# Kernel optimization log

Hardware: AMD Instinct MI355X
Metric: run time of the kernel (lower is better)

## Reference

```python
import jax, jax.numpy as jnp
import numpy as np
from jax import lax

B = 256; C_IN = 12; H = 84; W = 84
HID = 1024; NC = 16; NE = 512; EPC = 64
FLAT = 64 * 7 * 7  # encoder output size for 84x84 input


def setup_inputs() -> dict:
    key = jax.random.key(0)
    ks = jax.random.split(key, 16)
    s = 0.02
    inp = {
        "obs": jax.random.normal(ks[0], (B, C_IN, H, W), dtype=jnp.float32),
        "k1": jax.random.normal(ks[1], (32, C_IN, 8, 8), dtype=jnp.float32) * s,
        "cb1": jnp.zeros((32,), jnp.float32),
        "k2": jax.random.normal(ks[2], (64, 32, 4, 4), dtype=jnp.float32) * s,
        "cb2": jnp.zeros((64,), jnp.float32),
        "k3": jax.random.normal(ks[3], (64, 64, 3, 3), dtype=jnp.float32) * s,
        "cb3": jnp.zeros((64,), jnp.float32),
        "Wproj": jax.random.normal(ks[4], (FLAT, HID), dtype=jnp.float32) * s,
        "bproj": jnp.zeros((HID,), jnp.float32),
        "Wcat": jax.random.normal(ks[5], (HID, NC), dtype=jnp.float32) * s,
        "bcat": jnp.zeros((NC,), jnp.float32),
        "W1": jax.random.normal(ks[6], (NC, HID, HID // 2), dtype=jnp.float32) * s,
        "b1": jnp.zeros((NC, HID // 2), jnp.float32),
        "W2": jax.random.normal(ks[7], (NC, HID // 2, EPC), dtype=jnp.float32) * s,
        "b2": jnp.zeros((NC, EPC), jnp.float32),
        "mapping": jax.random.randint(ks[8], (NC, EPC), 0, NE, dtype=jnp.int64)
        if jax.config.jax_enable_x64 else jax.random.randint(ks[8], (NC, EPC), 0, NE, dtype=jnp.int32),
    }
    return inp


def _conv(x, k, b, stride):
    y = lax.conv_general_dilated(x, k, (stride, stride), "VALID",
                                 dimension_numbers=("NCHW", "OIHW", "NCHW"))
    return y + b[None, :, None, None]


def reference(obs, k1, cb1, k2, cb2, k3, cb3, Wproj, bproj, Wcat, bcat,
              W1, b1, W2, b2, mapping):
    # --- CNN encoder ---
    x = jax.nn.relu(_conv(obs, k1, cb1, 4))   # [B,32,20,20]
    x = jax.nn.relu(_conv(x, k2, cb2, 2))     # [B,64,9,9]
    x = jax.nn.relu(_conv(x, k3, cb3, 1))     # [B,64,7,7]
    feats = x.reshape(x.shape[0], -1)          # [B,3136]

    hidden = jax.nn.relu(feats @ Wproj + bproj)          # [B,HID]
    category_logits = hidden @ Wcat + bcat               # [B,NC]
    category_probs = jax.nn.softmax(category_logits, axis=-1)

    # --- batched per-category expert heads (fused) ---
    h1 = jax.nn.relu(jnp.einsum("bh,chm->bcm", hidden, W1) + b1)   # [B,NC,HID/2]
    local = jax.nn.sigmoid(jnp.einsum("bcm,cme->bce", h1, W2) + b2)  # [B,NC,EPC]
    weighted = category_probs[:, :, None] * local                    # [B,NC,EPC]

    # scatter-add into global expert buffer; mapping [NC,EPC] broadcasts to [B,NC,EPC]
    expert_probs = jnp.zeros((hidden.shape[0], NE), hidden.dtype)
    expert_probs = expert_probs.at[:, mapping].add(weighted)

    return category_logits, expert_probs, hidden
```

## Files before the change

### kernel.cpp

```cpp
#include <hip/hip_runtime.h>
#include <hip/hip_bf16.h>


#define B_    256
#define CIN   12
#define HH    84
#define WW    84
#define HID   1024
#define NC    16
#define NE    512
#define EPC   64
#define FLAT  3136

typedef short short8 __attribute__((ext_vector_type(8)));
typedef short short4_t __attribute__((ext_vector_type(4)));
typedef float f32x4 __attribute__((ext_vector_type(4)));

__device__ __forceinline__ short f2bf(float x) {
    unsigned int u = __float_as_uint(x);
    u = (u + 0x7FFFu + ((u >> 16) & 1u)) >> 16;
    return (short)u;
}

__global__ __launch_bounds__(256) void cast_k1_kernel(
        const float* __restrict__ k1, short* __restrict__ k1bf) {
    int i = blockIdx.x * 256 + threadIdx.x;
    if (i < 32 * 768) k1bf[i] = f2bf(k1[i]);
}

__global__ __launch_bounds__(256) void conv1_mfma_kernel(
        const float* __restrict__ obs, const short* __restrict__ k1bf,
        const float* __restrict__ cb1, float* __restrict__ x1) {
    const int tid = threadIdx.x;
    const int w = tid >> 6, l = tid & 63;
    const int lr = l & 15, g = l >> 4;
    const int mfb = blockIdx.x * 64 + w * 16;

    const int row_a = mfb + lr;
    const int b_a = row_a / 400;
    const int p_a = row_a % 400;
    const int oy = p_a / 20, ox = p_a % 20;
    const float* abase = obs + (size_t)b_a * (CIN * HH * WW) + (4 * oy) * WW + 4 * ox;
    const short* bb0 = k1bf + lr * 768;
    const short* bb1 = k1bf + (16 + lr) * 768;

    f32x4 acc0 = {0.f, 0.f, 0.f, 0.f}, acc1 = {0.f, 0.f, 0.f, 0.f};
    #pragma unroll 4
    for (int s = 0; s < 24; ++s) {
        const int idx = s * 4 + g;
        const int ic = idx >> 3, ky = idx & 7;
        const float* ap = abase + ic * (HH * WW) + ky * WW;
        float4 f0 = *(const float4*)ap;
        float4 f1 = *(const float4*)(ap + 4);
        short8 a;
        a[0] = f2bf(f0.x); a[1] = f2bf(f0.y); a[2] = f2bf(f0.z); a[3] = f2bf(f0.w);
        a[4] = f2bf(f1.x); a[5] = f2bf(f1.y); a[6] = f2bf(f1.z); a[7] = f2bf(f1.w);
        short8 b0 = *(const short8*)(bb0 + s * 32 + g * 8);
        short8 b1 = *(const short8*)(bb1 + s * 32 + g * 8);
        acc0 = __builtin_amdgcn_mfma_f32_16x16x32_bf16(a, b0, acc0, 0, 0, 0);
        acc1 = __builtin_amdgcn_mfma_f32_16x16x32_bf16(a, b1, acc1, 0, 0, 0);
    }
    #pragma unroll
    for (int r = 0; r < 4; ++r) {
        const int ro = mfb + g * 4 + r;
        const int b_o = ro / 400, p_o = ro % 400;
        float* xp = x1 + (size_t)b_o * 32 * 400 + p_o;
        xp[(size_t)lr * 400]        = fmaxf(acc0[r] + cb1[lr], 0.f);
        xp[(size_t)(16 + lr) * 400] = fmaxf(acc1[r] + cb1[16 + lr], 0.f);
    }
}

__global__ __launch_bounds__(288) void conv2_kernel(
        const float* __restrict__ x1, const float* __restrict__ k2,
        const float* __restrict__ cb2, float* __restrict__ x2) {
    __shared__ float slab[32][20][20];
    const int b = blockIdx.x, tid = threadIdx.x;
    const float* src = x1 + (size_t)b * 32 * 400;
    float4* s4 = (float4*)&slab[0][0][0];
    const float4* g4 = (const float4*)src;
    for (int l = tid; l < 3200; l += 288) s4[l] = g4[l];
    __syncthreads();

    const int ocp = tid / 9, oy = tid % 9;
    const int oc0 = 2 * ocp;
    float acc[2][9];
    #pragma unroll
    for (int o = 0; o < 2; ++o) {
        float bv = cb2[oc0 + o];
        #pragma unroll
        for (int i = 0; i < 9; ++i) acc[o][i] = bv;
    }
    for (int ic = 0; ic < 32; ++ic) {
        float wvv[2][16];
        const float* wp = k2 + oc0 * 512 + ic * 16;
        #pragma unroll
        for (int o = 0; o < 2; ++o)
            #pragma unroll
            for (int ky = 0; ky < 4; ++ky) {
                float4 t = *(const float4*)(wp + o * 512 + 4 * ky);
                wvv[o][4*ky] = t.x; wvv[o][4*ky+1] = t.y;
                wvv[o][4*ky+2] = t.z; wvv[o][4*ky+3] = t.w;
            }
        #pragma unroll
        for (int ky = 0; ky < 4; ++ky) {
            const int row = 2 * oy + ky;
            float rf[20];
            const float4* rp = (const float4*)&slab[ic][row][0];
            #pragma unroll
            for (int q = 0; q < 5; ++q) {
                float4 t = rp[q];
                rf[4*q] = t.x; rf[4*q+1] = t.y; rf[4*q+2] = t.z; rf[4*q+3] = t.w;
            }
            #pragma unroll
            for (int ox = 0; ox < 9; ++ox)
                #pragma unroll
                for (int kx = 0; kx < 4; ++kx) {
                    float v = rf[2 * ox + kx];
                    acc[0][ox] += v * wvv[0][4 * ky + kx];
                    acc[1][ox] += v * wvv[1][4 * ky + kx];
                }
        }
    }
    #pragma unroll
    for (int o = 0; o < 2; ++o) {
        float* dst = x2 + ((size_t)(b * 64 + oc0 + o) * 9 + oy) * 9;
        #pragma unroll
        for (int ox = 0; ox < 9; ++ox) dst[ox] = fmaxf(acc[o][ox], 0.f);
    }
}

__global__ __launch_bounds__(224) void conv3_kernel(
        const float* __restrict__ x2, const float* __restrict__ k3,
        const float* __restrict__ cb3, short* __restrict__ featsbf) {
    __shared__ float slab[64][9][12];
    const int b = blockIdx.x, tid = threadIdx.x;
    for (int l = tid; l < 64 * 9 * 12; l += 224) {
        int ic = l / 108, rest = l % 108, r = rest / 12, x = rest % 12;
        slab[ic][r][x] = (x < 9) ? x2[((size_t)(b * 64 + ic) * 9 + r) * 9 + x] : 0.f;
    }
    __syncthreads();

    const int ocp = tid / 7, oy = tid % 7;
    const int oc0 = 2 * ocp;
    float acc[2][7];
    #pragma unroll
    for (int o = 0; o < 2; ++o) {
        float bv = cb3[oc0 + o];
        #pragma unroll
        for (int i = 0; i < 7; ++i) acc[o][i] = bv;
    }
    for (int ic = 0; ic < 64; ++ic) {
        float wv2[2][9];
        const float* wp = k3 + oc0 * 576 + ic * 9;
        #pragma unroll
        for (int j = 0; j < 9; ++j) { wv2[0][j] = wp[j]; wv2[1][j] = wp[576 + j]; }
        #pragma unroll
        for (int ky = 0; ky < 3; ++ky) {
            const int row = oy + ky;
            float rf[12];
            const float4* rp = (const float4*)&slab[ic][row][0];
            #pragma unroll
            for (int q = 0; q < 3; ++q) {
                float4 t = rp[q];
                rf[4*q] = t.x; rf[4*q+1] = t.y; rf[4*q+2] = t.z; rf[4*q+3] = t.w;
            }
            #pragma unroll
            for (int ox = 0; ox < 7; ++ox)
                #pragma unroll
                for (int kx = 0; kx < 3; ++kx) {
                    float v = rf[ox + kx];
                    acc[0][ox] += v * wv2[0][3 * ky + kx];
                    acc[1][ox] += v * wv2[1][3 * ky + kx];
                }
        }
    }
    #pragma unroll
    for (int o = 0; o < 2; ++o) {
        short* dst = featsbf + (size_t)b * FLAT + (oc0 + o) * 49 + oy * 7;
        #pragma unroll
        for (int ox = 0; ox < 7; ++ox) dst[ox] = f2bf(fmaxf(acc[o][ox], 0.f));
    }
}

__global__ __launch_bounds__(256) void proj_mfma_kernel(
        const short* __restrict__ Abf, const float* __restrict__ W,
        float* __restrict__ accum4) {
    __shared__ __align__(16) short lbt[16][40];
    const int tid = threadIdx.x;
    const int w = tid >> 6, l = tid & 63, lr = l & 15, g = l >> 4;
    const int n0 = blockIdx.x * 16;
    const int kz = blockIdx.y;
    const int sb = kz * 24 + (kz < 2 ? kz : 2);
    const int ns = (kz < 2) ? 25 : 24;
    const int krp = tid >> 4, nn = tid & 15;

    f32x4 acc[4] = {};
    const short* arow[4];
    #pragma unroll
    for (int i = 0; i < 4; ++i)
        arow[i] = Abf + (size_t)(w * 64 + i * 16 + lr) * FLAT;

    for (int s = sb; s < sb + ns; ++s) {
        const int k0 = s * 32;
        {
            const float* wp = W + (size_t)(k0 + 2 * krp) * HID + n0 + nn;
            unsigned int lo = (unsigned short)f2bf(wp[0]);
            unsigned int hi = (unsigned short)f2bf(wp[HID]);
            *(unsigned int*)&lbt[nn][2 * krp] = lo | (hi << 16);
        }
        __syncthreads();
        short8 b = *(const short8*)&lbt[lr][g * 8];
        #pragma unroll
        for (int i = 0; i < 4; ++i) {
            short8 a = *(const short8*)(arow[i] + k0 + g * 8);
            acc[i] = __builtin_amdgcn_mfma_f32_16x16x32_bf16(a, b, acc[i], 0, 0, 0);
        }
        __syncthreads();
    }
    float* dst = accum4 + (size_t)kz * (B_ * HID);
    #pragma unroll
    for (int i = 0; i < 4; ++i)
        #pragma unroll
        for (int r = 0; r < 4; ++r)
            dst[(size_t)(w * 64 + i * 16 + g * 4 + r) * HID + n0 + lr] = acc[i][r];
}

__global__ __launch_bounds__(256) void proj_epi2_kernel(
        const float* __restrict__ accum4, const float* __restrict__ bproj,
        float* __restrict__ hidden, short* __restrict__ hbf) {
    const int i = blockIdx.x * 256 + threadIdx.x;
    float4 v = *(const float4*)&accum4[4 * i];
    #pragma unroll
    for (int kz = 1; kz < 4; ++kz) {
        float4 t = *(const float4*)&accum4[(size_t)kz * (B_ * HID) + 4 * i];
        v.x += t.x; v.y += t.y; v.z += t.z; v.w += t.w;
    }
    float4 bb = *(const float4*)&bproj[(4 * i) & (HID - 1)];
    float4 r;
    r.x = fmaxf(v.x + bb.x, 0.f); r.y = fmaxf(v.y + bb.y, 0.f);
    r.z = fmaxf(v.z + bb.z, 0.f); r.w = fmaxf(v.w + bb.w, 0.f);
    *(float4*)&hidden[4 * i] = r;
    short4_t h; h[0] = f2bf(r.x); h[1] = f2bf(r.y); h[2] = f2bf(r.z); h[3] = f2bf(r.w);
    *(short4_t*)&hbf[4 * i] = h;
}

__global__ __launch_bounds__(256) void cat_softmax_kernel(
        const float* __restrict__ hidden, const float* __restrict__ Wcat,
        const float* __restrict__ bcat, float* __restrict__ logits,
        float* __restrict__ probs) {
    __shared__ float red[256];
    __shared__ float lvals[16];
    const int b = blockIdx.x, tid = threadIdx.x;
    const int cc = tid & 15, kq = tid >> 4;
    const float* hrow = hidden + (size_t)b * HID;
    float p = 0.f;
    for (int t = 0; t < 64; ++t) {
        int k = kq * 64 + t;
        p += hrow[k] * Wcat[k * NC + cc];
    }
    red[tid] = p;
    __syncthreads();
    if (tid < 16) {
        float s = bcat[tid];
        #pragma unroll
        for (int q = 0; q < 16; ++q) s += red[q * 16 + tid];
        logits[b * NC + tid] = s;
        lvals[tid] = s;
    }
    __syncthreads();
    if (tid < 16) {
        float m = lvals[0];
        #pragma unroll
        for (int q = 1; q < 16; ++q) m = fmaxf(m, lvals[q]);
        float sum = 0.f;
        #pragma unroll
        for (int q = 0; q < 16; ++q) sum += expf(lvals[q] - m);
        probs[b * NC + tid] = expf(lvals[tid] - m) / sum;
    }
}

__global__ __launch_bounds__(256) void expert1_mfma_kernel(
        const short* __restrict__ Hbf, const float* __restrict__ W1,
        const float* __restrict__ b1, short* __restrict__ h1bf) {
    __shared__ __align__(16) short lbt[32][40];
    const int tid = threadIdx.x;
    const int w = tid >> 6, l = tid & 63, lr = l & 15, g = l >> 4;
    const int n0 = blockIdx.x * 32;
    const int c  = blockIdx.y;
    const float* Wc = W1 + (size_t)c * (HID * (HID / 2));

    f32x4 acc[4][2] = {};
    const short* arow[4];
    #pragma unroll
    for (int i = 0; i < 4; ++i)
        arow[i] = Hbf + (size_t)(w * 64 + i * 16 + lr) * HID;

    for (int s = 0; s < 32; ++s) {
        const int k0 = s * 32;
        #pragma unroll
        for (int it = 0; it < 2; ++it) {
            const int idx = tid + it * 256;
            const int krp = idx >> 5, nn = idx & 31;
            const float* wp = Wc + (size_t)(k0 + 2 * krp) * (HID / 2) + n0 + nn;
            unsigned int lo = (unsigned short)f2bf(wp[0]);
            unsigned int hi = (unsigned short)f2bf(wp[HID / 2]);
            *(unsigned int*)&lbt[nn][2 * krp] = lo | (hi << 16);
        }
        __syncthreads();
        short8 b0 = *(const short8*)&lbt[lr][g * 8];
        short8 b1v = *(const short8*)&lbt[16 + lr][g * 8];
        #pragma unroll
        for (int i = 0; i < 4; ++i) {
            short8 a = *(const short8*)(arow[i] + k0 + g * 8);
            acc[i][0] = __builtin_amdgcn_mfma_f32_16x16x32_bf16(a, b0, acc[i][0], 0, 0, 0);
            acc[i][1] = __builtin_amdgcn_mfma_f32_16x16x32_bf16(a, b1v, acc[i][1], 0, 0, 0);
        }
        __syncthreads();
    }
    #pragma unroll
    for (int i = 0; i < 4; ++i)
        #pragma unroll
        for (int j = 0; j < 2; ++j)
            #pragma unroll
            for (int r = 0; r < 4; ++r) {
                const int m = w * 64 + i * 16 + g * 4 + r;
                const int col = n0 + j * 16 + lr;
                float v = fmaxf(acc[i][j][r] + b1[c * (HID / 2) + col], 0.f);
                h1bf[((size_t)c * B_ + m) * (HID / 2) + col] = f2bf(v);
            }
}

__global__ __launch_bounds__(256) void expert2_mfma_kernel(
        const short* __restrict__ h1bf, const float* __restrict__ W2,
        const float* __restrict__ b2, const float* __restrict__ probs,
        const int* __restrict__ mapping, float* __restrict__ outexp) {
    __shared__ __align__(16) short lbt[64][40];
    const int tid = threadIdx.x;
    const int w = tid >> 6, l = tid & 63, lr = l & 15, g = l >> 4;
    const int mfb = blockIdx.x * 16;
    const int c = blockIdx.y;
    const float* Wc = W2 + (size_t)c * ((HID / 2) * EPC);
    const short* arow = h1bf + ((size_t)c * B_ + mfb + lr) * (HID / 2);

    f32x4 acc = {};
    for (int s = 0; s < 16; ++s) {
        const int k0 = s * 32;
        #pragma unroll
        for (int it = 0; it < 4; ++it) {
            const int idx = tid + it * 256;
            const int krp = idx >> 6, nn = idx & 63;
            const float* wp = Wc + (size_t)(k0 + 2 * krp) * EPC + nn;
            unsigned int lo = (unsigned short)f2bf(wp[0]);
            unsigned int hi = (unsigned short)f2bf(wp[EPC]);
            *(unsigned int*)&lbt[nn][2 * krp] = lo | (hi << 16);
        }
        __syncthreads();
        short8 b = *(const short8*)&lbt[w * 16 + lr][g * 8];
        short8 a = *(const short8*)(arow + k0 + g * 8);
        acc = __builtin_amdgcn_mfma_f32_16x16x32_bf16(a, b, acc, 0, 0, 0);
        __syncthreads();
    }
    const int e = w * 16 + lr;
    const float bb = b2[c * EPC + e];
    const int tgt = mapping[c * EPC + e];
    #pragma unroll
    for (int r = 0; r < 4; ++r) {
        const int m = mfb + g * 4 + r;
        const float lg = acc[r] + bb;
        const float v = probs[m * NC + c] / (1.f + expf(-lg));
        atomicAdd(&outexp[(size_t)m * NE + tgt], v);
    }
}

extern "C" void kernel_launch(void* const* d_in, const int* in_sizes, int n_in,
                              void* d_out, int out_size, void* d_ws, size_t ws_size,
                              hipStream_t stream) {
    const float* obs   = (const float*)d_in[0];
    const float* k1    = (const float*)d_in[1];
    const float* cb1   = (const float*)d_in[2];
    const float* k2    = (const float*)d_in[3];
    const float* cb2   = (const float*)d_in[4];
    const float* k3    = (const float*)d_in[5];
    const float* cb3   = (const float*)d_in[6];
    const float* Wproj = (const float*)d_in[7];
    const float* bproj = (const float*)d_in[8];
    const float* Wcat  = (const float*)d_in[9];
    const float* bcat  = (const float*)d_in[10];
    const float* W1    = (const float*)d_in[11];
    const float* b1    = (const float*)d_in[12];
    const float* W2    = (const float*)d_in[13];
    const float* b2    = (const float*)d_in[14];
    const int*   mapping = (const int*)d_in[15];

    float* out    = (float*)d_out;
    float* logits = out;
    float* outexp = out + B_ * NC;
    float* hidden = out + B_ * NC + B_ * NE;

    char* ws = (char*)d_ws;
    float* x1      = (float*)ws;
    float* accum4  = (float*)ws;
    short* h1bf    = (short*)(ws + 4194304);
    short* hidbf   = (short*)(ws + 8388608);
    float* x2      = (float*)(ws + 13107200);
    short* featsbf = (short*)(ws + 18415616);
    float* probs   = (float*)(ws + 20021248);
    short* k1bf    = (short*)(ws + 20037632);

    hipMemsetAsync(outexp, 0, (size_t)B_ * NE * sizeof(float), stream);

    cast_k1_kernel<<<dim3(96), 256, 0, stream>>>(k1, k1bf);
    conv1_mfma_kernel<<<dim3(1600), 256, 0, stream>>>(obs, k1bf, cb1, x1);
    conv2_kernel<<<dim3(B_), 288, 0, stream>>>(x1, k2, cb2, x2);
    conv3_kernel<<<dim3(B_), 224, 0, stream>>>(x2, k3, cb3, featsbf);
    proj_mfma_kernel<<<dim3(64, 4), 256, 0, stream>>>(featsbf, Wproj, accum4);
    proj_epi2_kernel<<<dim3(256), 256, 0, stream>>>(accum4, bproj, hidden, hidbf);
    cat_softmax_kernel<<<dim3(B_), 256, 0, stream>>>(hidden, Wcat, bcat, logits, probs);
    expert1_mfma_kernel<<<dim3(16, 16), 256, 0, stream>>>(hidbf, W1, b1, h1bf);
    expert2_mfma_kernel<<<dim3(16, 16), 256, 0, stream>>>(h1bf, W2, b2, probs, mapping, outexp);
}
```

Before: 408.8 us.

## Move all convs to MFMA with NHWC bf16 activations and pre-transposed bf16 weights

```diff
diff --git a/kernel.cpp b/kernel.cpp
--- a/kernel.cpp
+++ b/kernel.cpp
@@ -22,25 +22,64 @@
     return (short)u;
 }
 
-__global__ __launch_bounds__(256) void cast_k1_kernel(
-        const float* __restrict__ k1, short* __restrict__ k1bf) {
+__global__ __launch_bounds__(256) void prep_weights_kernel(
+        const float* __restrict__ k1, const float* __restrict__ k2,
+        const float* __restrict__ k3, short* __restrict__ k1bf,
+        short* __restrict__ k2t, short* __restrict__ k3t) {
     int i = blockIdx.x * 256 + threadIdx.x;
-    if (i < 32 * 768) k1bf[i] = f2bf(k1[i]);
-}
-
-__global__ __launch_bounds__(256) void conv1_mfma_kernel(
+    if (i < 24576) {
+        k1bf[i] = f2bf(k1[i]);
+    } else if (i < 24576 + 32768) {
+        int j = i - 24576;
+        int oc = j >> 9, rem = j & 511, tap = rem >> 5, ic = rem & 31;
+        k2t[j] = f2bf(k2[oc * 512 + ic * 16 + tap]);
+    } else if (i < 24576 + 32768 + 36864) {
+        int j = i - 57344;
+        int oc = j / 576, rem = j % 576, tap = rem >> 6, ic = rem & 63;
+        k3t[j] = f2bf(k3[oc * 576 + ic * 9 + tap]);
+    }
+}
+
+__global__ __launch_bounds__(256) void transpose_cast_kernel(
+        const float* __restrict__ src, short* __restrict__ dst,
+        int R, int C, long sbs, long dbs) {
+    __shared__ float tile[32][33];
+    const int c0 = blockIdx.x * 32, r0 = blockIdx.y * 32, z = blockIdx.z;
+    const int tx = threadIdx.x & 31, ty = threadIdx.x >> 5;
+    const float* s = src + (size_t)z * sbs;
+    short* d = dst + (size_t)z * dbs;
+    #pragma unroll
+    for (int it = 0; it < 4; ++it)
+        tile[ty + it * 8][tx] = s[(size_t)(r0 + ty + it * 8) * C + c0 + tx];
+    __syncthreads();
+    #pragma unroll
+    for (int it = 0; it < 4; ++it) {
+        int j = ty + it * 8;
+        d[(size_t)(c0 + j) * R + r0 + tx] = f2bf(tile[tx][j]);
+    }
+}
+
+__global__ __launch_bounds__(448) void conv1_mfma_kernel(
         const float* __restrict__ obs, const short* __restrict__ k1bf,
-        const float* __restrict__ cb1, float* __restrict__ x1) {
+        const float* __restrict__ cb1, short* __restrict__ x1bf) {
+    __shared__ short slab[CIN][24][88];
+    const int oyq = blockIdx.x, b = blockIdx.y;
     const int tid = threadIdx.x;
-    const int w = tid >> 6, l = tid & 63;
-    const int lr = l & 15, g = l >> 4;
-    const int mfb = blockIdx.x * 64 + w * 16;
-
-    const int row_a = mfb + lr;
-    const int b_a = row_a / 400;
-    const int p_a = row_a % 400;
-    const int oy = p_a / 20, ox = p_a % 20;
-    const float* abase = obs + (size_t)b_a * (CIN * HH * WW) + (4 * oy) * WW + 4 * ox;
+
+    const float* src = obs + (size_t)b * (CIN * HH * WW) + (20 * oyq) * WW;
+    for (int l = tid; l < CIN * 24 * 21; l += 448) {
+        int ic = l / 504, rem = l % 504, r = rem / 21, c4 = rem % 21;
+        float4 f = *(const float4*)(src + (size_t)ic * (HH * WW) + r * WW + 4 * c4);
+        short4_t v;
+        v[0] = f2bf(f.x); v[1] = f2bf(f.y); v[2] = f2bf(f.z); v[3] = f2bf(f.w);
+        *(short4_t*)&slab[ic][r][4 * c4] = v;
+    }
+    __syncthreads();
+
+    const int w = tid >> 6, l = tid & 63, lr = l & 15, g = l >> 4;
+    const int p = w * 16 + lr;
+    const int pw = (p < 100) ? p : 99;
+    const int oy_l = pw / 20, ox = pw % 20;
     const short* bb0 = k1bf + lr * 768;
     const short* bb1 = k1bf + (16 + lr) * 768;
 
@@ -49,199 +88,130 @@
     for (int s = 0; s < 24; ++s) {
         const int idx = s * 4 + g;
         const int ic = idx >> 3, ky = idx & 7;
-        const float* ap = abase + ic * (HH * WW) + ky * WW;
-        float4 f0 = *(const float4*)ap;
-        float4 f1 = *(const float4*)(ap + 4);
+        const short* ap = &slab[ic][4 * oy_l + ky][4 * ox];
         short8 a;
-        a[0] = f2bf(f0.x); a[1] = f2bf(f0.y); a[2] = f2bf(f0.z); a[3] = f2bf(f0.w);
-        a[4] = f2bf(f1.x); a[5] = f2bf(f1.y); a[6] = f2bf(f1.z); a[7] = f2bf(f1.w);
+        *(short4_t*)&a       = *(const short4_t*)ap;
+        *((short4_t*)&a + 1) = *(const short4_t*)(ap + 4);
         short8 b0 = *(const short8*)(bb0 + s * 32 + g * 8);
         short8 b1 = *(const short8*)(bb1 + s * 32 + g * 8);
         acc0 = __builtin_amdgcn_mfma_f32_16x16x32_bf16(a, b0, acc0, 0, 0, 0);
         acc1 = __builtin_amdgcn_mfma_f32_16x16x32_bf16(a, b1, acc1, 0, 0, 0);
     }
+    const float c0v = cb1[lr], c1v = cb1[16 + lr];
     #pragma unroll
     for (int r = 0; r < 4; ++r) {
-        const int ro = mfb + g * 4 + r;
-        const int b_o = ro / 400, p_o = ro % 400;
-        float* xp = x1 + (size_t)b_o * 32 * 400 + p_o;
-        xp[(size_t)lr * 400]        = fmaxf(acc0[r] + cb1[lr], 0.f);
-        xp[(size_t)(16 + lr) * 400] = fmaxf(acc1[r] + cb1[16 + lr], 0.f);
-    }
-}
-
-__global__ __launch_bounds__(288) void conv2_kernel(
-        const float* __restrict__ x1, const float* __restrict__ k2,
-        const float* __restrict__ cb2, float* __restrict__ x2) {
-    __shared__ float slab[32][20][20];
-    const int b = blockIdx.x, tid = threadIdx.x;
-    const float* src = x1 + (size_t)b * 32 * 400;
-    float4* s4 = (float4*)&slab[0][0][0];
-    const float4* g4 = (const float4*)src;
-    for (int l = tid; l < 3200; l += 288) s4[l] = g4[l];
-    __syncthreads();
-
-    const int ocp = tid / 9, oy = tid % 9;
-    const int oc0 = 2 * ocp;
-    float acc[2][9];
-    #pragma unroll
-    for (int o = 0; o < 2; ++o) {
-        float bv = cb2[oc0 + o];
-        #pragma unroll
-        for (int i = 0; i < 9; ++i) acc[o][i] = bv;
-    }
-    for (int ic = 0; ic < 32; ++ic) {
-        float wvv[2][16];
-        const float* wp = k2 + oc0 * 512 + ic * 16;
-        #pragma unroll
-        for (int o = 0; o < 2; ++o)
-            #pragma unroll
-            for (int ky = 0; ky < 4; ++ky) {
-                float4 t = *(const float4*)(wp + o * 512 + 4 * ky);
-                wvv[o][4*ky] = t.x; wvv[o][4*ky+1] = t.y;
-                wvv[o][4*ky+2] = t.z; wvv[o][4*ky+3] = t.w;
-            }
-        #pragma unroll
-        for (int ky = 0; ky < 4; ++ky) {
-            const int row = 2 * oy + ky;
-            float rf[20];
-            const float4* rp = (const float4*)&slab[ic][row][0];
-            #pragma unroll
-            for (int q = 0; q < 5; ++q) {
-                float4 t = rp[q];
-                rf[4*q] = t.x; rf[4*q+1] = t.y; rf[4*q+2] = t.z; rf[4*q+3] = t.w;
-            }
-            #pragma unroll
-            for (int ox = 0; ox < 9; ++ox)
-                #pragma unroll
-                for (int kx = 0; kx < 4; ++kx) {
-                    float v = rf[2 * ox + kx];
-                    acc[0][ox] += v * wvv[0][4 * ky + kx];
-                    acc[1][ox] += v * wvv[1][4 * ky + kx];
-                }
-        }
-    }
-    #pragma unroll
-    for (int o = 0; o < 2; ++o) {
-        float* dst = x2 + ((size_t)(b * 64 + oc0 + o) * 9 + oy) * 9;
-        #pragma unroll
-        for (int ox = 0; ox < 9; ++ox) dst[ox] = fmaxf(acc[o][ox], 0.f);
-    }
-}
-
-__global__ __launch_bounds__(224) void conv3_kernel(
-        const float* __restrict__ x2, const float* __restrict__ k3,
+        const int ro = w * 16 + g * 4 + r;
+        if (ro < 100) {
+            const int oy_g = 5 * oyq + ro / 20, ox_g = ro % 20;
+            short* dst = x1bf + ((size_t)(b * 20 + oy_g) * 20 + ox_g) * 32;
+            dst[lr]      = f2bf(fmaxf(acc0[r] + c0v, 0.f));
+            dst[16 + lr] = f2bf(fmaxf(acc1[r] + c1v, 0.f));
+        }
+    }
+}
+
+__global__ __launch_bounds__(64) void conv2_mfma_kernel(
+        const short* __restrict__ x1bf, const short* __restrict__ k2t,
+        const float* __restrict__ cb2, short* __restrict__ x2bf) {
+    const int l = threadIdx.x, lr = l & 15, g = l >> 4;
+    const int mfb = blockIdx.x * 16;
+    const int ro = mfb + lr;
+    const int b = ro / 81, pp = ro % 81, oy = pp / 9, ox = pp % 9;
+    const short* abase = x1bf + (size_t)b * 12800;
+
+    f32x4 acc[4] = {};
+    #pragma unroll 4
+    for (int s = 0; s < 16; ++s) {
+        const int ky = s >> 2, kx = s & 3;
+        short8 a = *(const short8*)(abase +
+            ((size_t)((2 * oy + ky) * 20 + 2 * ox + kx)) * 32 + g * 8);
+        #pragma unroll
+        for (int nf = 0; nf < 4; ++nf) {
+            short8 bv = *(const short8*)(k2t + (size_t)(nf * 16 + lr) * 512 + s * 32 + g * 8);
+            acc[nf] = __builtin_amdgcn_mfma_f32_16x16x32_bf16(a, bv, acc[nf], 0, 0, 0);
+        }
+    }
+    #pragma unroll
+    for (int nf = 0; nf < 4; ++nf) {
+        const int col = nf * 16 + lr;
+        const float bb = cb2[col];
+        #pragma unroll
+        for (int r = 0; r < 4; ++r) {
+            const int roo = mfb + g * 4 + r;
+            x2bf[(size_t)roo * 64 + col] = f2bf(fmaxf(acc[nf][r] + bb, 0.f));
+        }
+    }
+}
+
+__global__ __launch_bounds__(64) void conv3_mfma_kernel(
+        const short* __restrict__ x2bf, const short* __restrict__ k3t,
         const float* __restrict__ cb3, short* __restrict__ featsbf) {
-    __shared__ float slab[64][9][12];
-    const int b = blockIdx.x, tid = threadIdx.x;
-    for (int l = tid; l < 64 * 9 * 12; l += 224) {
-        int ic = l / 108, rest = l % 108, r = rest / 12, x = rest % 12;
-        slab[ic][r][x] = (x < 9) ? x2[((size_t)(b * 64 + ic) * 9 + r) * 9 + x] : 0.f;
-    }
-    __syncthreads();
-
-    const int ocp = tid / 7, oy = tid % 7;
-    const int oc0 = 2 * ocp;
-    float acc[2][7];
-    #pragma unroll
-    for (int o = 0; o < 2; ++o) {
-        float bv = cb3[oc0 + o];
-        #pragma unroll
-        for (int i = 0; i < 7; ++i) acc[o][i] = bv;
-    }
-    for (int ic = 0; ic < 64; ++ic) {
-        float wv2[2][9];
-        const float* wp = k3 + oc0 * 576 + ic * 9;
-        #pragma unroll
-        for (int j = 0; j < 9; ++j) { wv2[0][j] = wp[j]; wv2[1][j] = wp[576 + j]; }
-        #pragma unroll
-        for (int ky = 0; ky < 3; ++ky) {
-            const int row = oy + ky;
-            float rf[12];
-            const float4* rp = (const float4*)&slab[ic][row][0];
-            #pragma unroll
-            for (int q = 0; q < 3; ++q) {
-                float4 t = rp[q];
-                rf[4*q] = t.x; rf[4*q+1] = t.y; rf[4*q+2] = t.z; rf[4*q+3] = t.w;
-            }
-            #pragma unroll
-            for (int ox = 0; ox < 7; ++ox)
-                #pragma unroll
-                for (int kx = 0; kx < 3; ++kx) {
-                    float v = rf[ox + kx];
-                    acc[0][ox] += v * wv2[0][3 * ky + kx];
-                    acc[1][ox] += v * wv2[1][3 * ky + kx];
-                }
-        }
-    }
-    #pragma unroll
-    for (int o = 0; o < 2; ++o) {
-        short* dst = featsbf + (size_t)b * FLAT + (oc0 + o) * 49 + oy * 7;
-        #pragma unroll
-        for (int ox = 0; ox < 7; ++ox) dst[ox] = f2bf(fmaxf(acc[o][ox], 0.f));
-    }
-}
-
-__global__ __launch_bounds__(256) void proj_mfma_kernel(
-        const short* __restrict__ Abf, const float* __restrict__ W,
-        float* __restrict__ accum4) {
-    __shared__ __align__(16) short lbt[16][40];
-    const int tid = threadIdx.x;
-    const int w = tid >> 6, l = tid & 63, lr = l & 15, g = l >> 4;
-    const int n0 = blockIdx.x * 16;
-    const int kz = blockIdx.y;
-    const int sb = kz * 24 + (kz < 2 ? kz : 2);
-    const int ns = (kz < 2) ? 25 : 24;
-    const int krp = tid >> 4, nn = tid & 15;
+    const int l = threadIdx.x, lr = l & 15, g = l >> 4;
+    const int mfb = blockIdx.x * 16;
+    const int ro = mfb + lr;
+    const int b = ro / 49, pp = ro % 49, oy = pp / 7, ox = pp % 7;
+    const short* abase = x2bf + (size_t)b * 5184;
 
     f32x4 acc[4] = {};
-    const short* arow[4];
-    #pragma unroll
-    for (int i = 0; i < 4; ++i)
-        arow[i] = Abf + (size_t)(w * 64 + i * 16 + lr) * FLAT;
-
-    for (int s = sb; s < sb + ns; ++s) {
-        const int k0 = s * 32;
-        {
-            const float* wp = W + (size_t)(k0 + 2 * krp) * HID + n0 + nn;
-            unsigned int lo = (unsigned short)f2bf(wp[0]);
-            unsigned int hi = (unsigned short)f2bf(wp[HID]);
-            *(unsigned int*)&lbt[nn][2 * krp] = lo | (hi << 16);
-        }
-        __syncthreads();
-        short8 b = *(const short8*)&lbt[lr][g * 8];
-        #pragma unroll
-        for (int i = 0; i < 4; ++i) {
-            short8 a = *(const short8*)(arow[i] + k0 + g * 8);
-            acc[i] = __builtin_amdgcn_mfma_f32_16x16x32_bf16(a, b, acc[i], 0, 0, 0);
-        }
-        __syncthreads();
-    }
-    float* dst = accum4 + (size_t)kz * (B_ * HID);
-    #pragma unroll
-    for (int i = 0; i < 4; ++i)
-        #pragma unroll
-        for (int r = 0; r < 4; ++r)
-            dst[(size_t)(w * 64 + i * 16 + g * 4 + r) * HID + n0 + lr] = acc[i][r];
-}
-
-__global__ __launch_bounds__(256) void proj_epi2_kernel(
-        const float* __restrict__ accum4, const float* __restrict__ bproj,
-        float* __restrict__ hidden, short* __restrict__ hbf) {
-    const int i = blockIdx.x * 256 + threadIdx.x;
-    float4 v = *(const float4*)&accum4[4 * i];
-    #pragma unroll
-    for (int kz = 1; kz < 4; ++kz) {
-        float4 t = *(const float4*)&accum4[(size_t)kz * (B_ * HID) + 4 * i];
-        v.x += t.x; v.y += t.y; v.z += t.z; v.w += t.w;
-    }
-    float4 bb = *(const float4*)&bproj[(4 * i) & (HID - 1)];
-    float4 r;
-    r.x = fmaxf(v.x + bb.x, 0.f); r.y = fmaxf(v.y + bb.y, 0.f);
-    r.z = fmaxf(v.z + bb.z, 0.f); r.w = fmaxf(v.w + bb.w, 0.f);
-    *(float4*)&hidden[4 * i] = r;
-    short4_t h; h[0] = f2bf(r.x); h[1] = f2bf(r.y); h[2] = f2bf(r.z); h[3] = f2bf(r.w);
-    *(short4_t*)&hbf[4 * i] = h;
+    #pragma unroll 4
+    for (int s = 0; s < 18; ++s) {
+        const int tap = s >> 1, ich = s & 1;
+        const int ky = tap / 3, kx = tap % 3;
+        short8 a = *(const short8*)(abase +
+            ((size_t)((oy + ky) * 9 + ox + kx)) * 64 + ich * 32 + g * 8);
+        #pragma unroll
+        for (int nf = 0; nf < 4; ++nf) {
+            short8 bv = *(const short8*)(k3t + (size_t)(nf * 16 + lr) * 576 + s * 32 + g * 8);
+            acc[nf] = __builtin_amdgcn_mfma_f32_16x16x32_bf16(a, bv, acc[nf], 0, 0, 0);
+        }
+    }
+    #pragma unroll
+    for (int nf = 0; nf < 4; ++nf) {
+        const int col = nf * 16 + lr;
+        const float bb = cb3[col];
+        #pragma unroll
+        for (int r = 0; r < 4; ++r) {
+            const int roo = mfb + g * 4 + r;
+            const int b_o = roo / 49, p_o = roo % 49;
+            featsbf[(size_t)b_o * FLAT + col * 49 + p_o] =
+                f2bf(fmaxf(acc[nf][r] + bb, 0.f));
+        }
+    }
+}
+
+__global__ __launch_bounds__(64) void proj_mfma_kernel(
+        const short* __restrict__ Abf, const short* __restrict__ Wt,
+        const float* __restrict__ bproj, float* __restrict__ hidden,
+        short* __restrict__ hbf) {
+    const int l = threadIdx.x, lr = l & 15, g = l >> 4;
+    const int n0 = blockIdx.x * 16, m0 = blockIdx.y * 32;
+    const short* a0 = Abf + (size_t)(m0 + lr) * FLAT;
+    const short* a1 = Abf + (size_t)(m0 + 16 + lr) * FLAT;
+    const short* br = Wt + (size_t)(n0 + lr) * FLAT;
+
+    f32x4 acc0 = {}, acc1 = {};
+    #pragma unroll 4
+    for (int s = 0; s < 98; ++s) {
+        const int k = s * 32 + g * 8;
+        short8 bv = *(const short8*)(br + k);
+        short8 av0 = *(const short8*)(a0 + k);
+        short8 av1 = *(const short8*)(a1 + k);
+        acc0 = __builtin_amdgcn_mfma_f32_16x16x32_bf16(av0, bv, acc0, 0, 0, 0);
+        acc1 = __builtin_amdgcn_mfma_f32_16x16x32_bf16(av1, bv, acc1, 0, 0, 0);
+    }
+    const int col = n0 + lr;
+    const float bb = bproj[col];
+    #pragma unroll
+    for (int r = 0; r < 4; ++r) {
+        const int m = m0 + g * 4 + r;
+        float v = fmaxf(acc0[r] + bb, 0.f);
+        hidden[(size_t)m * HID + col] = v;
+        hbf[(size_t)m * HID + col] = f2bf(v);
+        const int m2 = m + 16;
+        float v2 = fmaxf(acc1[r] + bb, 0.f);
+        hidden[(size_t)m2 * HID + col] = v2;
+        hbf[(size_t)m2 * HID + col] = f2bf(v2);
+    }
 }
 
 __global__ __launch_bounds__(256) void cat_softmax_kernel(
@@ -279,96 +249,76 @@
     }
 }
 
-__global__ __launch_bounds__(256) void expert1_mfma_kernel(
-        const short* __restrict__ Hbf, const float* __restrict__ W1,
+__global__ __launch_bounds__(64) void expert1_mfma_kernel(
+        const short* __restrict__ Hbf, const short* __restrict__ W1t,
         const float* __restrict__ b1, short* __restrict__ h1bf) {
-    __shared__ __align__(16) short lbt[32][40];
-    const int tid = threadIdx.x;
-    const int w = tid >> 6, l = tid & 63, lr = l & 15, g = l >> 4;
-    const int n0 = blockIdx.x * 32;
-    const int c  = blockIdx.y;
-    const float* Wc = W1 + (size_t)c * (HID * (HID / 2));
+    const int l = threadIdx.x, lr = l & 15, g = l >> 4;
+    const int n0 = blockIdx.x * 32, m0 = blockIdx.y * 64, c = blockIdx.z;
+    const short* ar[4];
+    #pragma unroll
+    for (int i = 0; i < 4; ++i) ar[i] = Hbf + (size_t)(m0 + i * 16 + lr) * HID;
+    const short* br0 = W1t + (size_t)c * (512 * HID) + (size_t)(n0 + lr) * HID;
+    const short* br1 = br0 + 16 * HID;
 
     f32x4 acc[4][2] = {};
-    const short* arow[4];
-    #pragma unroll
-    for (int i = 0; i < 4; ++i)
-        arow[i] = Hbf + (size_t)(w * 64 + i * 16 + lr) * HID;
-
+    #pragma unroll 2
     for (int s = 0; s < 32; ++s) {
-        const int k0 = s * 32;
-        #pragma unroll
-        for (int it = 0; it < 2; ++it) {
-            const int idx = tid + it * 256;
-            const int krp = idx >> 5, nn = idx & 31;
-            const float* wp = Wc + (size_t)(k0 + 2 * krp) * (HID / 2) + n0 + nn;
-            unsigned int lo = (unsigned short)f2bf(wp[0]);
-            unsigned int hi = (unsigned short)f2bf(wp[HID / 2]);
-            *(unsigned int*)&lbt[nn][2 * krp] = lo | (hi << 16);
-        }
-        __syncthreads();
-        short8 b0 = *(const short8*)&lbt[lr][g * 8];
-        short8 b1v = *(const short8*)&lbt[16 + lr][g * 8];
+        const int k = s * 32 + g * 8;
+        short8 b0 = *(const short8*)(br0 + k);
+        short8 b1v = *(const short8*)(br1 + k);
         #pragma unroll
         for (int i = 0; i < 4; ++i) {
-            short8 a = *(const short8*)(arow[i] + k0 + g * 8);
+            short8 a = *(const short8*)(ar[i] + k);
             acc[i][0] = __builtin_amdgcn_mfma_f32_16x16x32_bf16(a, b0, acc[i][0], 0, 0, 0);
             acc[i][1] = __builtin_amdgcn_mfma_f32_16x16x32_bf16(a, b1v, acc[i][1], 0, 0, 0);
         }
-        __syncthreads();
-    }
-    #pragma unroll
-    for (int i = 0; i < 4; ++i)
-        #pragma unroll
-        for (int j = 0; j < 2; ++j)
+    }
+    #pragma unroll
+    for (int j = 0; j < 2; ++j) {
+        const int col = n0 + j * 16 + lr;
+        const float bb = b1[c * 512 + col];
+        #pragma unroll
+        for (int i = 0; i < 4; ++i)
             #pragma unroll
             for (int r = 0; r < 4; ++r) {
-                const int m = w * 64 + i * 16 + g * 4 + r;
-                const int col = n0 + j * 16 + lr;
-                float v = fmaxf(acc[i][j][r] + b1[c * (HID / 2) + col], 0.f);
-                h1bf[((size_t)c * B_ + m) * (HID / 2) + col] = f2bf(v);
+                const int m = m0 + i * 16 + g * 4 + r;
+                h1bf[((size_t)c * B_ + m) * 512 + col] =
+                    f2bf(fmaxf(acc[i][j][r] + bb, 0.f));
             }
-}
-
-__global__ __launch_bounds__(256) void expert2_mfma_kernel(
-        const short* __restrict__ h1bf, const float* __restrict__ W2,
+    }
+}
+
+__global__ __launch_bounds__(64) void expert2_mfma_kernel(
+        const short* __restrict__ h1bf, const short* __restrict__ W2t,
         const float* __restrict__ b2, const float* __restrict__ probs,
         const int* __restrict__ mapping, float* __restrict__ outexp) {
-    __shared__ __align__(16) short lbt[64][40];
-    const int tid = threadIdx.x;
-    const int w = tid >> 6, l = tid & 63, lr = l & 15, g = l >> 4;
-    const int mfb = blockIdx.x * 16;
-    const int c = blockIdx.y;
-    const float* Wc = W2 + (size_t)c * ((HID / 2) * EPC);
-    const short* arow = h1bf + ((size_t)c * B_ + mfb + lr) * (HID / 2);
-
-    f32x4 acc = {};
+    const int l = threadIdx.x, lr = l & 15, g = l >> 4;
+    const int mfb = blockIdx.x * 16, c = blockIdx.y;
+    const short* ar = h1bf + ((size_t)c * B_ + mfb + lr) * 512;
+    const short* wb = W2t + (size_t)c * (EPC * 512);
+
+    f32x4 acc[4] = {};
+    #pragma unroll 4
     for (int s = 0; s < 16; ++s) {
-        const int k0 = s * 32;
-        #pragma unroll
-        for (int it = 0; it < 4; ++it) {
-            const int idx = tid + it * 256;
-            const int krp = idx >> 6, nn = idx & 63;
-            const float* wp = Wc + (size_t)(k0 + 2 * krp) * EPC + nn;
-            unsigned int lo = (unsigned short)f2bf(wp[0]);
-            unsigned int hi = (unsigned short)f2bf(wp[EPC]);
-            *(unsigned int*)&lbt[nn][2 * krp] = lo | (hi << 16);
-        }
-        __syncthreads();
-        short8 b = *(const short8*)&lbt[w * 16 + lr][g * 8];
-        short8 a = *(const short8*)(arow + k0 + g * 8);
-        acc = __builtin_amdgcn_mfma_f32_16x16x32_bf16(a, b, acc, 0, 0, 0);
-        __syncthreads();
-    }
-    const int e = w * 16 + lr;
-    const float bb = b2[c * EPC + e];
-    const int tgt = mapping[c * EPC + e];
-    #pragma unroll
-    for (int r = 0; r < 4; ++r) {
-        const int m = mfb + g * 4 + r;
-        const float lg = acc[r] + bb;
-        const float v = probs[m * NC + c] / (1.f + expf(-lg));
-        atomicAdd(&outexp[(size_t)m * NE + tgt], v);
+        const int k = s * 32 + g * 8;
+        short8 a = *(const short8*)(ar + k);
+        #pragma unroll
+        for (int nf = 0; nf < 4; ++nf) {
+            short8 bv = *(const short8*)(wb + (size_t)(nf * 16 + lr) * 512 + k);
+            acc[nf] = __builtin_amdgcn_mfma_f32_16x16x32_bf16(a, bv, acc[nf], 0, 0, 0);
+        }
+    }
+    #pragma unroll
+    for (int nf = 0; nf < 4; ++nf) {
+        const int e = nf * 16 + lr;
+        const float bb = b2[c * EPC + e];
+        const int tgt = mapping[c * EPC + e];
+        #pragma unroll
+        for (int r = 0; r < 4; ++r) {
+            const int m = mfb + g * 4 + r;
+            const float v = probs[m * NC + c] / (1.f + expf(-(acc[nf][r] + bb)));
+            atomicAdd(&outexp[(size_t)m * NE + tgt], v);
+        }
     }
 }
 
@@ -398,24 +348,34 @@
     float* hidden = out + B_ * NC + B_ * NE;
 
     char* ws = (char*)d_ws;
-    float* x1      = (float*)ws;
-    float* accum4  = (float*)ws;
-    short* h1bf    = (short*)(ws + 4194304);
-    short* hidbf   = (short*)(ws + 8388608);
-    float* x2      = (float*)(ws + 13107200);
-    short* featsbf = (short*)(ws + 18415616);
-    float* probs   = (float*)(ws + 20021248);
-    short* k1bf    = (short*)(ws + 20037632);
+    short* x1bf    = (short*)ws;
+    short* Wprojt  = (short*)ws;
+    short* W1t     = (short*)ws;
+    short* W2t     = (short*)ws;
+    short* x2bf    = (short*)(ws + 6553600);
+    short* featsbf = (short*)(ws + 9207808);
+    short* hidbf   = (short*)(ws + 16777216);
+    float* probs   = (float*)(ws + 17301504);
+    short* k1bf    = (short*)(ws + 17317888);
+    short* k2t     = (short*)(ws + 17367040);
+    short* k3t     = (short*)(ws + 17432576);
+    short* h1bf    = (short*)(ws + 17506304);
 
     hipMemsetAsync(outexp, 0, (size_t)B_ * NE * sizeof(float), stream);
 
-    cast_k1_kernel<<<dim3(96), 256, 0, stream>>>(k1, k1bf);
-    conv1_mfma_kernel<<<dim3(1600), 256, 0, stream>>>(obs, k1bf, cb1, x1);
-    conv2_kernel<<<dim3(B_), 288, 0, stream>>>(x1, k2, cb2, x2);
-    conv3_kernel<<<dim3(B_), 224, 0, stream>>>(x2, k3, cb3, featsbf);
-    proj_mfma_kernel<<<dim3(64, 4), 256, 0, stream>>>(featsbf, Wproj, accum4);
-    proj_epi2_kernel<<<dim3(256), 256, 0, stream>>>(accum4, bproj, hidden, hidbf);
+    prep_weights_kernel<<<dim3(368), 256, 0, stream>>>(k1, k2, k3, k1bf, k2t, k3t);
+    conv1_mfma_kernel<<<dim3(4, B_), 448, 0, stream>>>(obs, k1bf, cb1, x1bf);
+    conv2_mfma_kernel<<<dim3(1296), 64, 0, stream>>>(x1bf, k2t, cb2, x2bf);
+    transpose_cast_kernel<<<dim3(32, 98, 1), 256, 0, stream>>>(
+        Wproj, Wprojt, FLAT, HID, 0, 0);
+    conv3_mfma_kernel<<<dim3(784), 64, 0, stream>>>(x2bf, k3t, cb3, featsbf);
+    proj_mfma_kernel<<<dim3(64, 8), 64, 0, stream>>>(featsbf, Wprojt, bproj, hidden, hidbf);
     cat_softmax_kernel<<<dim3(B_), 256, 0, stream>>>(hidden, Wcat, bcat, logits, probs);
-    expert1_mfma_kernel<<<dim3(16, 16), 256, 0, stream>>>(hidbf, W1, b1, h1bf);
-    expert2_mfma_kernel<<<dim3(16, 16), 256, 0, stream>>>(h1bf, W2, b2, probs, mapping, outexp);
-}
+    transpose_cast_kernel<<<dim3(16, 32, 16), 256, 0, stream>>>(
+        W1, W1t, HID, 512, (long)HID * 512, (long)HID * 512);
+    expert1_mfma_kernel<<<dim3(16, 4, 16), 64, 0, stream>>>(hidbf, W1t, b1, h1bf);
+    transpose_cast_kernel<<<dim3(2, 16, 16), 256, 0, stream>>>(
+        W2, W2t, 512, EPC, (long)512 * EPC, (long)512 * EPC);
+    expert2_mfma_kernel<<<dim3(16, 16), 64, 0, stream>>>(
+        h1bf, W2t, b2, probs, mapping, outexp);
+}
```

After: 373.7 us. 1.09x faster.
